# Optimization experiments

Measured on AMD Instinct MI355X. Metric: run time of the kernel, lower is better.

## Reference

```python
import jax, jax.numpy as jnp
import numpy as np

# MANO prior contact vertex indices (f1+f2+f3+f4+f5+f0 from CMap_loss3)
_F1 = [697,698,699,700,712,713,714,715,737,738,739,740,741,743,744,745,746,748,749,750,753,754,755,756,757,758,759,760,761,762,763,764,765,766,767,768]
_F2 = [46,47,48,49,164,165,166,167,194,195,223,237,238,280,281,298,301,317,320,323,324,325,326,327,328,329,330,331,332,333,340,341,342,343,344,345,346,347,348,349,350,351,352,353,354,355]
_F3 = [356,357,358,359,375,376,386,387,396,397,402,403,413,429,433,434,435,436,437,438,439,440,441,442,443,444,452,453,454,455,456,459,460,461,462,463,464,465,466,467]
_F4 = [468,469,470,471,484,485,486,496,497,506,507,513,514,524,545,546,547,548,549,550,551,552,553,555,563,564,565,566,567,570,572,573,574,575,576,577,578]
_F5 = [580,581,582,583,600,601,602,614,615,624,625,630,631,641,663,664,665,666,667,668,670,672,680,681,682,683,684,686,687,688,689,690,691,692,693,694,695]
_F0 = [73,96,98,99,772,774,775,777]
PRIOR_IDX = np.array(_F1 + _F2 + _F3 + _F4 + _F5 + _F0, dtype=np.int32)


def _sqdist(a, b):
    # a: [B,N,3], b: [B,M,3] -> squared distances [B,N,M] via ||a||^2+||b||^2-2ab
    a2 = jnp.sum(a * a, -1)          # [B,N]
    b2 = jnp.sum(b * b, -1)          # [B,M]
    ab = jnp.einsum('bnd,bmd->bnm', a, b)
    return jnp.maximum(a2[:, :, None] + b2[:, None, :] - 2.0 * ab, 0.0)


def _knn1(src, trg):
    # nearest neighbor (K=1): squared dists + indices, like pytorch3d knn_points
    d2 = _sqdist(src, trg)           # [B,N,M]
    return jnp.min(d2, -1), jnp.argmin(d2, -1)


def _verts_normals(verts, faces):
    # area-weighted vertex normals (pytorch3d verts_normals_packed)
    v0 = verts[:, faces[:, 0]]       # [B,F,3]
    v1 = verts[:, faces[:, 1]]
    v2 = verts[:, faces[:, 2]]
    fn = jnp.cross(v1 - v0, v2 - v0)
    vn = jnp.zeros_like(verts)
    vn = vn.at[:, faces[:, 0]].add(fn).at[:, faces[:, 1]].add(fn).at[:, faces[:, 2]].add(fn)
    return vn / (jnp.linalg.norm(vn, axis=-1, keepdims=True) + 1e-12)


def setup_inputs() -> dict:
    key = jax.random.key(0)
    ks = jax.random.split(key, 8)
    B, N1, V, F, Z, P = 64, 8192, 778, 1538, 64, 61
    scale = 0.1  # keep points in a 0.1 box so contact thresholds (0.005/0.01) fire
    return {
        'obj_xyz': jax.random.uniform(ks[0], (B, N1, 3), jnp.float32) * scale,
        'recon_xyz': jax.random.uniform(ks[1], (B, V, 3), jnp.float32) * scale,
        'gt_xyz': jax.random.uniform(ks[2], (B, V, 3), jnp.float32) * scale,
        'mean': jax.random.normal(ks[3], (B, Z), jnp.float32),
        'log_var': jax.random.normal(ks[4], (B, Z), jnp.float32),
        'recon_param': jax.random.normal(ks[5], (B, P), jnp.float32),
        'x_param': jax.random.normal(ks[6], (B, P), jnp.float32),
        'faces': jax.random.randint(ks[7], (F, 3), 0, V, jnp.int32),
    }


def reference(obj_xyz, recon_xyz, gt_xyz, mean, log_var, recon_param, x_param, faces):
    B = obj_xyz.shape[0]
    fB = jnp.float32(B)

    # KNN from object points to gt / reconstructed hand (squared dists)
    d_gt, _ = _knn1(obj_xyz, gt_xyz)            # [B,N1]
    d_rec, idx_rec = _knn1(obj_xyz, recon_xyz)  # [B,N1], [B,N1]

    # param loss: MSE sum / B
    param_loss = jnp.sum((recon_param - x_param) ** 2) / fB

    # CVAE loss: chamfer (point_reduction='sum', batch_reduction='mean') + KLD
    d2 = _sqdist(recon_xyz, gt_xyz)             # [B,778,778]
    recon_loss = jnp.mean(jnp.sum(jnp.min(d2, -1), -1)) + jnp.mean(jnp.sum(jnp.min(d2, -2), -1))
    KLD = -0.5 * jnp.sum(1.0 + log_var - mean ** 2 - jnp.exp(log_var)) / fB * 10.0
    cvae_loss = recon_loss + KLD

    # CMap_loss3: obj NN distance to prior hand contact verts, masked by cmap
    cmap = d_rec < 0.01 ** 2                    # [B,N1] bool
    prior = recon_xyz[:, PRIOR_IDX, :]          # [B,222,3]
    obj_CD, _ = _knn1(obj_xyz, prior)           # [B,N1]
    n_points = jnp.sum(cmap).astype(jnp.float32)
    cmap_loss = 3000.0 * jnp.sum(jnp.where(cmap, obj_CD, 0.0)) / (fB * n_points)

    # CMap consistency: contact-map overlap ratio
    recon_cmap = jnp.sqrt(d_rec) < 0.005
    gt_cmap = jnp.sqrt(d_gt) < 0.005
    gt_cnum = jnp.sum(gt_cmap).astype(jnp.float32) + 0.0001
    consistency_loss = -5.0 * jnp.sum(recon_cmap & gt_cmap).astype(jnp.float32) / gt_cnum

    # inter-penetration: gather NN hand verts/normals, sign of dot, masked dist sum
    vn = _verts_normals(recon_xyz, faces)                               # [B,778,3]
    nn_v = jnp.take_along_axis(recon_xyz, idx_rec[..., None], axis=1)   # [B,N1,3]
    nn_n = jnp.take_along_axis(vn, idx_rec[..., None], axis=1)          # [B,N1,3]
    interior = jnp.sum((nn_v - obj_xyz) * nn_n, -1) > 0                 # [B,N1]
    penetr_loss = 100.0 * jnp.sum(jnp.where(interior, d_rec, 0.0)) / fB

    a, b, c, d, e = 1.0, 0.1, 1000.0, 10.0, 10.0
    loss = a * cvae_loss + b * param_loss + c * cmap_loss + d * consistency_loss + e * penetr_loss
    return loss
```

## Files before the change

### kernel.cpp

```cpp
#include <hip/hip_runtime.h>
#include <math.h>

#define NB     64
#define N1V    8192
#define NPTS   (NB * N1V)
#define NV     778
#define NVP    780
#define NQ     195
#define SEG1Q  51
#define NFACE  1538
#define NZ     64
#define NPAR   61
#define NPRIOR 204
#define PPT    8
#define BIAS   0.0625f

#define REC_BLOCKS 256
#define GT_BLOCKS  256
#define CH_BLOCKS  128
#define NROLE_BLOCKS (REC_BLOCKS + GT_BLOCKS + CH_BLOCKS)
#define CMB_BLOCKS 64

#define BATCH_F4 2352
#define ACC_OFF (NB * BATCH_F4 * 4)
#define RC_OFF  (ACC_OFF + 16)
#define GC_OFF  (RC_OFF + NPTS / 32)

__device__ __constant__ int c_prior[NPRIOR] = {
  697,698,699,700,712,713,714,715,737,738,739,740,741,743,744,745,746,748,749,750,
  753,754,755,756,757,758,759,760,761,762,763,764,765,766,767,768,
  46,47,48,49,164,165,166,167,194,195,223,237,238,280,281,298,301,317,320,323,
  324,325,326,327,328,329,330,331,332,333,340,341,342,343,344,345,346,347,348,349,
  350,351,352,353,354,355,
  356,357,358,359,375,376,386,387,396,397,402,403,413,429,433,434,435,436,437,438,
  439,440,441,442,443,444,452,453,454,455,456,459,460,461,462,463,464,465,466,467,
  468,469,470,471,484,485,486,496,497,506,507,513,514,524,545,546,547,548,549,550,
  551,552,553,555,563,564,565,566,567,570,572,573,574,575,576,577,578,
  580,581,582,583,600,601,602,614,615,624,625,630,631,641,663,664,665,666,667,668,
  670,672,680,681,682,683,684,686,687,688,689,690,691,692,693,694,695,
  73,96,98,99,772,774,775,777
};

__global__ __launch_bounds__(256) void k_prep(const float* __restrict__ recon,
                                              const float* __restrict__ gt,
                                              const int* __restrict__ faces,
                                              float4* __restrict__ ws4,
                                              float* __restrict__ acc) {
    int b = blockIdx.x, tid = threadIdx.x;
    if (b == 0 && tid < 16) acc[tid] = 0.0f;
    __shared__ float4 s_r[NV];
    __shared__ float s_vnx[NV], s_vny[NV], s_vnz[NV];
    __shared__ unsigned int s_bm[25];
    __shared__ unsigned short s_pre[26];
    __shared__ unsigned short s_perm[NV];

    if (tid < 25) s_bm[tid] = 0u;
    __syncthreads();
    if (tid < NPRIOR) {
        int v = c_prior[tid];
        atomicOr(&s_bm[v >> 5], 1u << (v & 31));
    }
    const float* rb = recon + (size_t)b * NV * 3;
    const float* gb = gt    + (size_t)b * NV * 3;
    float4* gt4   = ws4 + (size_t)b * BATCH_F4;
    float4* rec4p = gt4 + NVP;
    float4* nrm4p = rec4p + NVP;
    for (int j = tid; j < NV; j += 256) {
        float x = rb[3*j], y = rb[3*j+1], z = rb[3*j+2];
        s_r[j] = make_float4(x, y, z, x*x + y*y + z*z + BIAS);
        x = gb[3*j]; y = gb[3*j+1]; z = gb[3*j+2];
        gt4[j] = make_float4(x, y, z, x*x + y*y + z*z);
        s_vnx[j] = 0.0f; s_vny[j] = 0.0f; s_vnz[j] = 0.0f;
    }
    if (tid < 2) gt4[NV + tid] = make_float4(0.f, 0.f, 0.f, 1e30f);
    __syncthreads();
    if (tid == 0) {
        unsigned int run = 0;
        for (int w = 0; w < 25; ++w) { s_pre[w] = (unsigned short)run; run += __popc(s_bm[w]); }
        s_pre[25] = (unsigned short)run;
    }
    __syncthreads();
    for (int j = tid; j < NV; j += 256) {
        int w = j >> 5;
        unsigned int below = s_bm[w] & ((1u << (j & 31)) - 1u);
        int rank = s_pre[w] + __popc(below);
        bool member = (s_bm[w] >> (j & 31)) & 1u;
        int pos = member ? rank : (NPRIOR + (j - rank));
        s_perm[pos] = (unsigned short)j;
    }
    for (int f = tid; f < NFACE; f += 256) {
        int i0 = faces[3*f], i1 = faces[3*f+1], i2 = faces[3*f+2];
        float4 p0 = s_r[i0], p1 = s_r[i1], p2 = s_r[i2];
        float e1x = p1.x - p0.x, e1y = p1.y - p0.y, e1z = p1.z - p0.z;
        float e2x = p2.x - p0.x, e2y = p2.y - p0.y, e2z = p2.z - p0.z;
        float fx = e1y * e2z - e1z * e2y;
        float fy = e1z * e2x - e1x * e2z;
        float fz = e1x * e2y - e1y * e2x;
        atomicAdd(&s_vnx[i0], fx); atomicAdd(&s_vny[i0], fy); atomicAdd(&s_vnz[i0], fz);
        atomicAdd(&s_vnx[i1], fx); atomicAdd(&s_vny[i1], fy); atomicAdd(&s_vnz[i1], fz);
        atomicAdd(&s_vnx[i2], fx); atomicAdd(&s_vny[i2], fy); atomicAdd(&s_vnz[i2], fz);
    }
    __syncthreads();
    for (int j = tid; j < NVP; j += 256) {
        if (j < NV) {
            int src = s_perm[j];
            rec4p[j] = s_r[src];
            float x = s_vnx[src], y = s_vny[src], z = s_vnz[src];
            float inv = 1.0f / (sqrtf(x*x + y*y + z*z) + 1e-12f);
            nrm4p[j] = make_float4(x * inv, y * inv, z * inv, 0.0f);
        } else {
            rec4p[j] = make_float4(0.f, 0.f, 0.f, 1e30f);
            nrm4p[j] = make_float4(0.f, 0.f, 1.f, 0.0f);
        }
    }
}

#define LOAD_PTS(ob)                                                          \
    const float4* ob4 = (const float4*)((ob) + (size_t)tid * 24);             \
    float4 q0 = ob4[0], q1 = ob4[1], q2 = ob4[2],                             \
           q3 = ob4[3], q4 = ob4[4], q5 = ob4[5];                             \
    float px[PPT], py[PPT], pz[PPT];                                          \
    px[0]=q0.x; py[0]=q0.y; pz[0]=q0.z;  px[1]=q0.w; py[1]=q1.x; pz[1]=q1.y;  \
    px[2]=q1.z; py[2]=q1.w; pz[2]=q2.x;  px[3]=q2.y; py[3]=q2.z; pz[3]=q2.w;  \
    px[4]=q3.x; py[4]=q3.y; pz[4]=q3.z;  px[5]=q3.w; py[5]=q4.x; pz[5]=q4.y;  \
    px[6]=q4.z; py[6]=q4.w; pz[6]=q5.x;  px[7]=q5.y; py[7]=q5.z; pz[7]=q5.w;

__global__ __launch_bounds__(256) void k_fused(const float* __restrict__ obj,
                                               const float4* __restrict__ ws4,
                                               float* __restrict__ acc,
                                               unsigned char* __restrict__ rcA,
                                               unsigned char* __restrict__ gcA) {
    __shared__ float4 s_t[NVP];
    __shared__ float s_red[3];
    int tid = threadIdx.x;
    int blk = blockIdx.x;

    if (blk < REC_BLOCKS) {
        int b = blk >> 2, chunk = blk & 3;
        const float4* base = ws4 + (size_t)b * BATCH_F4;
        const float4* rec4p = base + NVP;
        const float4* nrm4p = base + 2 * NVP;
        for (int j = tid; j < NVP; j += 256) s_t[j] = rec4p[j];
        if (tid < 3) s_red[tid] = 0.0f;
        __syncthreads();

        const float* ob = obj + ((size_t)b * N1V + (size_t)chunk * 2048) * 3;
        LOAD_PTS(ob)
        float nax[PPT], nay[PPT], naz[PPT], m[PPT];
        int q[PPT];
#pragma unroll
        for (int i = 0; i < PPT; ++i) {
            nax[i] = -2.0f * px[i]; nay[i] = -2.0f * py[i]; naz[i] = -2.0f * pz[i];
            m[i] = 3.4e38f; q[i] = 0;
        }
        float mp[PPT];
#pragma unroll 1
        for (int jq = 0; jq < SEG1Q; ++jq) {
            int j = 4 * jq;
            float4 t0 = s_t[j], t1 = s_t[j+1], t2 = s_t[j+2], t3 = s_t[j+3];
#pragma unroll
            for (int i = 0; i < PPT; ++i) {
                float d0 = fmaf(nax[i], t0.x, fmaf(nay[i], t0.y, fmaf(naz[i], t0.z, t0.w)));
                float d1 = fmaf(nax[i], t1.x, fmaf(nay[i], t1.y, fmaf(naz[i], t1.z, t1.w)));
                float d2 = fmaf(nax[i], t2.x, fmaf(nay[i], t2.y, fmaf(naz[i], t2.z, t2.w)));
                float d3 = fmaf(nax[i], t3.x, fmaf(nay[i], t3.y, fmaf(naz[i], t3.z, t3.w)));
                float mn = fminf(fminf(fminf(d0, d1), fminf(d2, d3)), m[i]);
                q[i] = (mn < m[i]) ? jq : q[i];
                m[i] = mn;
            }
        }
#pragma unroll
        for (int i = 0; i < PPT; ++i) mp[i] = m[i];
#pragma unroll 1
        for (int jq = SEG1Q; jq < NQ; ++jq) {
            int j = 4 * jq;
            float4 t0 = s_t[j], t1 = s_t[j+1], t2 = s_t[j+2], t3 = s_t[j+3];
#pragma unroll
            for (int i = 0; i < PPT; ++i) {
                float d0 = fmaf(nax[i], t0.x, fmaf(nay[i], t0.y, fmaf(naz[i], t0.z, t0.w)));
                float d1 = fmaf(nax[i], t1.x, fmaf(nay[i], t1.y, fmaf(naz[i], t1.z, t1.w)));
                float d2 = fmaf(nax[i], t2.x, fmaf(nay[i], t2.y, fmaf(naz[i], t2.z, t2.w)));
                float d3 = fmaf(nax[i], t3.x, fmaf(nay[i], t3.y, fmaf(naz[i], t3.z, t3.w)));
                float mn = fminf(fminf(fminf(d0, d1), fminf(d2, d3)), m[i]);
                q[i] = (mn < m[i]) ? jq : q[i];
                m[i] = mn;
            }
        }
        float lS_cmap = 0.0f, lN_cmap = 0.0f, lS_pen = 0.0f;
        unsigned int rcbits = 0;
#pragma unroll
        for (int i = 0; i < PPT; ++i) {
            float a2 = px[i]*px[i] + py[i]*py[i] + pz[i]*pz[i];
            float drec = fmaxf(a2 + (m[i]  - BIAS), 0.0f);
            float dpri = fmaxf(a2 + (mp[i] - BIAS), 0.0f);
            bool cm = drec < 1e-4f;
            bool rc = sqrtf(drec) < 0.005f;
            if (cm) { lS_cmap += dpri; lN_cmap += 1.0f; }
            if (rc) rcbits |= (1u << i);
            int jr = 4 * q[i];
            float4 t0 = s_t[jr], t1 = s_t[jr+1], t2 = s_t[jr+2], t3 = s_t[jr+3];
            float d0 = fmaf(nax[i], t0.x, fmaf(nay[i], t0.y, fmaf(naz[i], t0.z, t0.w)));
            float d1 = fmaf(nax[i], t1.x, fmaf(nay[i], t1.y, fmaf(naz[i], t1.z, t1.w)));
            float d2 = fmaf(nax[i], t2.x, fmaf(nay[i], t2.y, fmaf(naz[i], t2.z, t2.w)));
            float d3 = fmaf(nax[i], t3.x, fmaf(nay[i], t3.y, fmaf(naz[i], t3.z, t3.w)));
            float mmin = fminf(fminf(d0, d1), fminf(d2, d3));
            int off = (d0 == mmin) ? 0 : ((d1 == mmin) ? 1 : ((d2 == mmin) ? 2 : 3));
            int jstar = jr + off;
            float4 tS = s_t[jstar];
            float4 nr = nrm4p[jstar];
            float ddot = (tS.x - px[i]) * nr.x + (tS.y - py[i]) * nr.y
                       + (tS.z - pz[i]) * nr.z;
            if (ddot > 0.0f) lS_pen += drec;
        }
        rcA[(size_t)blk * 256 + tid] = (unsigned char)rcbits;
        atomicAdd(&s_red[0], lS_cmap);
        atomicAdd(&s_red[1], lN_cmap);
        atomicAdd(&s_red[2], lS_pen);
        __syncthreads();
        if (tid == 0) atomicAdd(&acc[3], s_red[0]);
        if (tid == 1) atomicAdd(&acc[4], s_red[1]);
        if (tid == 2) atomicAdd(&acc[7], s_red[2]);
        return;
    }

    if (blk < REC_BLOCKS + GT_BLOCKS) {
        int r = blk - REC_BLOCKS;
        int b = r >> 2, chunk = r & 3;
        const float4* gt4v = ws4 + (size_t)b * BATCH_F4;
        for (int j = tid; j < NVP; j += 256) s_t[j] = gt4v[j];
        if (tid == 0) s_red[0] = 0.0f;
        __syncthreads();

        const float* ob = obj + ((size_t)b * N1V + (size_t)chunk * 2048) * 3;
        LOAD_PTS(ob)
        float nax[PPT], nay[PPT], naz[PPT], mgt[PPT];
#pragma unroll
        for (int i = 0; i < PPT; ++i) {
            nax[i] = -2.0f * px[i]; nay[i] = -2.0f * py[i]; naz[i] = -2.0f * pz[i];
            mgt[i] = 3.4e38f;
        }
#pragma unroll 1
        for (int jq = 0; jq < NQ; ++jq) {
            int j = 4 * jq;
            float4 t0 = s_t[j], t1 = s_t[j+1], t2 = s_t[j+2], t3 = s_t[j+3];
#pragma unroll
            for (int i = 0; i < PPT; ++i) {
                float d0 = fmaf(nax[i], t0.x, fmaf(nay[i], t0.y, fmaf(naz[i], t0.z, t0.w)));
                float d1 = fmaf(nax[i], t1.x, fmaf(nay[i], t1.y, fmaf(naz[i], t1.z, t1.w)));
                float d2 = fmaf(nax[i], t2.x, fmaf(nay[i], t2.y, fmaf(naz[i], t2.z, t2.w)));
                float d3 = fmaf(nax[i], t3.x, fmaf(nay[i], t3.y, fmaf(naz[i], t3.z, t3.w)));
                mgt[i] = fminf(fminf(mgt[i], fminf(d0, d1)), fminf(d2, d3));
            }
        }
        float lN_gt = 0.0f;
        unsigned int gcbits = 0;
#pragma unroll
        for (int i = 0; i < PPT; ++i) {
            float a2 = px[i]*px[i] + py[i]*py[i] + pz[i]*pz[i];
            float dgt = fmaxf(a2 + mgt[i], 0.0f);
            if (sqrtf(dgt) < 0.005f) { lN_gt += 1.0f; gcbits |= (1u << i); }
        }
        gcA[(size_t)r * 256 + tid] = (unsigned char)gcbits;
        atomicAdd(&s_red[0], lN_gt);
        __syncthreads();
        if (tid == 0) atomicAdd(&acc[5], s_red[0]);
        return;
    }

    {
        int c   = blk - (REC_BLOCKS + GT_BLOCKS);
        int b   = c >> 1;
        int dir = c & 1;
        const float4* base = ws4 + (size_t)b * BATCH_F4;
        const float4* srcv = dir ? base : (base + NVP);
        const float4* tgtv = dir ? (base + NVP) : base;
        for (int j = tid; j < NVP; j += 256) s_t[j] = tgtv[j];
        if (tid == 0) s_red[0] = 0.0f;
        __syncthreads();

        const int CPT = 4;
        float nax[CPT], nay[CPT], naz[CPT], a2[CPT], m[CPT];
        bool valid[CPT];
#pragma unroll
        for (int k = 0; k < CPT; ++k) {
            int p = tid + 256 * k;
            valid[k] = (p < NV);
            float4 s = srcv[valid[k] ? p : 0];
            nax[k] = -2.0f * s.x; nay[k] = -2.0f * s.y; naz[k] = -2.0f * s.z;
            a2[k] = s.w;
            m[k] = 3.4e38f;
        }
#pragma unroll 1
        for (int j = 0; j < NVP; j += 4) {
            float4 t0 = s_t[j], t1 = s_t[j+1], t2 = s_t[j+2], t3 = s_t[j+3];
#pragma unroll
            for (int k = 0; k < CPT; ++k) {
                float d0 = fmaf(nax[k], t0.x, fmaf(nay[k], t0.y, fmaf(naz[k], t0.z, t0.w)));
                float d1 = fmaf(nax[k], t1.x, fmaf(nay[k], t1.y, fmaf(naz[k], t1.z, t1.w)));
                float d2 = fmaf(nax[k], t2.x, fmaf(nay[k], t2.y, fmaf(naz[k], t2.z, t2.w)));
                float d3 = fmaf(nax[k], t3.x, fmaf(nay[k], t3.y, fmaf(naz[k], t3.z, t3.w)));
                m[k] = fminf(fminf(m[k], fminf(d0, d1)), fminf(d2, d3));
            }
        }
        float local = 0.0f;
#pragma unroll
        for (int k = 0; k < CPT; ++k)
            if (valid[k]) local += fmaxf(a2[k] + m[k] - BIAS, 0.0f);
        atomicAdd(&s_red[0], local);
        __syncthreads();
        if (tid == 0) atomicAdd(&acc[2], s_red[0]);
    }
}

__global__ __launch_bounds__(256) void k_combine(float* __restrict__ acc,
                                                 const unsigned int* __restrict__ rcW,
                                                 const unsigned int* __restrict__ gcW,
                                                 const float* __restrict__ mean,
                                                 const float* __restrict__ log_var,
                                                 const float* __restrict__ rp,
                                                 const float* __restrict__ xp,
                                                 float* __restrict__ out) {
    int blk = blockIdx.x, tid = threadIdx.x;
    __shared__ float s_red[2];
    __shared__ unsigned int s_ticket;
    if (tid < 2) s_red[tid] = 0.0f;
    __syncthreads();
    int idx = blk * 256 + tid;
    unsigned int rc = rcW[idx], gc = gcW[idx];
    float cnt = (float)__popc(rc & gc);
    atomicAdd(&s_red[0], cnt);
    __syncthreads();
    if (tid == 0) atomicAdd(&acc[6], s_red[0]);
    __threadfence();
    if (tid == 0) s_ticket = atomicAdd((unsigned int*)&acc[15], 1u);
    __syncthreads();

    if (s_ticket == CMB_BLOCKS - 1) {
        if (tid < 2) s_red[tid] = 0.0f;
        __syncthreads();
        float s_param = 0.0f, s_kld = 0.0f;
        for (int i = tid; i < NB * NPAR; i += 256) {
            float d = rp[i] - xp[i];
            s_param += d * d;
        }
        for (int i = tid; i < NB * NZ; i += 256) {
            float m = mean[i], lv = log_var[i];
            s_kld += 1.0f + lv - m * m - expf(lv);
        }
        atomicAdd(&s_red[0], s_param);
        atomicAdd(&s_red[1], s_kld);
        __syncthreads();
        if (tid == 0) {
            const float fB = 64.0f;
            float a2v = atomicAdd(&acc[2], 0.0f);
            float a3  = atomicAdd(&acc[3], 0.0f);
            float a4  = atomicAdd(&acc[4], 0.0f);
            float a5  = atomicAdd(&acc[5], 0.0f);
            float a6  = atomicAdd(&acc[6], 0.0f);
            float a7  = atomicAdd(&acc[7], 0.0f);
            float param_loss  = s_red[0] / fB;
            float KLD         = -0.5f * s_red[1] / fB * 10.0f;
            float recon_loss  = a2v / fB;
            float cmap_loss   = 3000.0f * a3 / (fB * a4);
            float consistency = -5.0f * a6 / (a5 + 0.0001f);
            float penetr      = 100.0f * a7 / fB;
            out[0] = (recon_loss + KLD) + 0.1f * param_loss + 1000.0f * cmap_loss
                   + 10.0f * consistency + 10.0f * penetr;
        }
    }
}

extern "C" void kernel_launch(void* const* d_in, const int* in_sizes, int n_in,
                              void* d_out, int out_size, void* d_ws, size_t ws_size,
                              hipStream_t stream) {
    (void)in_sizes; (void)n_in; (void)out_size; (void)ws_size;
    const float* obj     = (const float*)d_in[0];
    const float* recon   = (const float*)d_in[1];
    const float* gt      = (const float*)d_in[2];
    const float* mean    = (const float*)d_in[3];
    const float* log_var = (const float*)d_in[4];
    const float* rp      = (const float*)d_in[5];
    const float* xp      = (const float*)d_in[6];
    const int*   faces   = (const int*)d_in[7];
    float4* ws4 = (float4*)d_ws;
    float* acc  = (float*)d_ws + ACC_OFF;
    unsigned char* rcA = (unsigned char*)((float*)d_ws + RC_OFF);
    unsigned char* gcA = (unsigned char*)((float*)d_ws + GC_OFF);
    float* out  = (float*)d_out;

    k_prep   <<<NB,           256, 0, stream>>>(recon, gt, faces, ws4, acc);
    k_fused  <<<NROLE_BLOCKS, 256, 0, stream>>>(obj, ws4, acc, rcA, gcA);
    k_combine<<<CMB_BLOCKS,   256, 0, stream>>>(acc, (const unsigned int*)rcA,
                                                (const unsigned int*)gcA,
                                                mean, log_var, rp, xp, out);
}
```

Measured before the change: 197.4 us.

## Fuse prep into main kernel and replace global atomics with per-block partials

Removes the separate prep kernel. Each role block now builds its own permuted recon, gt or chamfer target table, and the rec blocks recompute face normals in shared memory. Global float atomics and the ticketed combine are replaced by per-block partial sums that a single-block tail kernel reduces. This drops one launch and the workspace round-trip. In exchange, normal computation is repeated four times per batch and shared memory per block grows, which may reduce occupancy.

```diff
diff --git a/kernel.cpp b/kernel.cpp
--- a/kernel.cpp
+++ b/kernel.cpp
@@ -18,13 +18,11 @@
 #define REC_BLOCKS 256
 #define GT_BLOCKS  256
 #define CH_BLOCKS  128
-#define NROLE_BLOCKS (REC_BLOCKS + GT_BLOCKS + CH_BLOCKS)
-#define CMB_BLOCKS 64
-
-#define BATCH_F4 2352
-#define ACC_OFF (NB * BATCH_F4 * 4)
-#define RC_OFF  (ACC_OFF + 16)
-#define GC_OFF  (RC_OFF + NPTS / 32)
+#define NROLE (REC_BLOCKS + GT_BLOCKS + CH_BLOCKS)
+
+#define PART_OFF 0
+#define RC_OFF   (NROLE * 4)
+#define GC_OFF   (RC_OFF + 16384)
 
 __device__ __constant__ int c_prior[NPRIOR] = {
   697,698,699,700,712,713,714,715,737,738,739,740,741,743,744,745,746,748,749,750,
@@ -41,80 +39,6 @@
   73,96,98,99,772,774,775,777
 };
 
-__global__ __launch_bounds__(256) void k_prep(const float* __restrict__ recon,
-                                              const float* __restrict__ gt,
-                                              const int* __restrict__ faces,
-                                              float4* __restrict__ ws4,
-                                              float* __restrict__ acc) {
-    int b = blockIdx.x, tid = threadIdx.x;
-    if (b == 0 && tid < 16) acc[tid] = 0.0f;
-    __shared__ float4 s_r[NV];
-    __shared__ float s_vnx[NV], s_vny[NV], s_vnz[NV];
-    __shared__ unsigned int s_bm[25];
-    __shared__ unsigned short s_pre[26];
-    __shared__ unsigned short s_perm[NV];
-
-    if (tid < 25) s_bm[tid] = 0u;
-    __syncthreads();
-    if (tid < NPRIOR) {
-        int v = c_prior[tid];
-        atomicOr(&s_bm[v >> 5], 1u << (v & 31));
-    }
-    const float* rb = recon + (size_t)b * NV * 3;
-    const float* gb = gt    + (size_t)b * NV * 3;
-    float4* gt4   = ws4 + (size_t)b * BATCH_F4;
-    float4* rec4p = gt4 + NVP;
-    float4* nrm4p = rec4p + NVP;
-    for (int j = tid; j < NV; j += 256) {
-        float x = rb[3*j], y = rb[3*j+1], z = rb[3*j+2];
-        s_r[j] = make_float4(x, y, z, x*x + y*y + z*z + BIAS);
-        x = gb[3*j]; y = gb[3*j+1]; z = gb[3*j+2];
-        gt4[j] = make_float4(x, y, z, x*x + y*y + z*z);
-        s_vnx[j] = 0.0f; s_vny[j] = 0.0f; s_vnz[j] = 0.0f;
-    }
-    if (tid < 2) gt4[NV + tid] = make_float4(0.f, 0.f, 0.f, 1e30f);
-    __syncthreads();
-    if (tid == 0) {
-        unsigned int run = 0;
-        for (int w = 0; w < 25; ++w) { s_pre[w] = (unsigned short)run; run += __popc(s_bm[w]); }
-        s_pre[25] = (unsigned short)run;
-    }
-    __syncthreads();
-    for (int j = tid; j < NV; j += 256) {
-        int w = j >> 5;
-        unsigned int below = s_bm[w] & ((1u << (j & 31)) - 1u);
-        int rank = s_pre[w] + __popc(below);
-        bool member = (s_bm[w] >> (j & 31)) & 1u;
-        int pos = member ? rank : (NPRIOR + (j - rank));
-        s_perm[pos] = (unsigned short)j;
-    }
-    for (int f = tid; f < NFACE; f += 256) {
-        int i0 = faces[3*f], i1 = faces[3*f+1], i2 = faces[3*f+2];
-        float4 p0 = s_r[i0], p1 = s_r[i1], p2 = s_r[i2];
-        float e1x = p1.x - p0.x, e1y = p1.y - p0.y, e1z = p1.z - p0.z;
-        float e2x = p2.x - p0.x, e2y = p2.y - p0.y, e2z = p2.z - p0.z;
-        float fx = e1y * e2z - e1z * e2y;
-        float fy = e1z * e2x - e1x * e2z;
-        float fz = e1x * e2y - e1y * e2x;
-        atomicAdd(&s_vnx[i0], fx); atomicAdd(&s_vny[i0], fy); atomicAdd(&s_vnz[i0], fz);
-        atomicAdd(&s_vnx[i1], fx); atomicAdd(&s_vny[i1], fy); atomicAdd(&s_vnz[i1], fz);
-        atomicAdd(&s_vnx[i2], fx); atomicAdd(&s_vny[i2], fy); atomicAdd(&s_vnz[i2], fz);
-    }
-    __syncthreads();
-    for (int j = tid; j < NVP; j += 256) {
-        if (j < NV) {
-            int src = s_perm[j];
-            rec4p[j] = s_r[src];
-            float x = s_vnx[src], y = s_vny[src], z = s_vnz[src];
-            float inv = 1.0f / (sqrtf(x*x + y*y + z*z) + 1e-12f);
-            nrm4p[j] = make_float4(x * inv, y * inv, z * inv, 0.0f);
-        } else {
-            rec4p[j] = make_float4(0.f, 0.f, 0.f, 1e30f);
-            nrm4p[j] = make_float4(0.f, 0.f, 1.f, 0.0f);
-        }
-    }
-}
-
 #define LOAD_PTS(ob)                                                          \
     const float4* ob4 = (const float4*)((ob) + (size_t)tid * 24);             \
     float4 q0 = ob4[0], q1 = ob4[1], q2 = ob4[2],                             \
@@ -125,23 +49,79 @@
     px[4]=q3.x; py[4]=q3.y; pz[4]=q3.z;  px[5]=q3.w; py[5]=q4.x; pz[5]=q4.y;  \
     px[6]=q4.z; py[6]=q4.w; pz[6]=q5.x;  px[7]=q5.y; py[7]=q5.z; pz[7]=q5.w;
 
-__global__ __launch_bounds__(256) void k_fused(const float* __restrict__ obj,
-                                               const float4* __restrict__ ws4,
-                                               float* __restrict__ acc,
-                                               unsigned char* __restrict__ rcA,
-                                               unsigned char* __restrict__ gcA) {
+__global__ __launch_bounds__(256) void k_all(const float* __restrict__ obj,
+                                             const float* __restrict__ recon,
+                                             const float* __restrict__ gt,
+                                             const int* __restrict__ faces,
+                                             float* __restrict__ part,
+                                             unsigned char* __restrict__ rcA,
+                                             unsigned char* __restrict__ gcA) {
     __shared__ float4 s_t[NVP];
-    __shared__ float s_red[3];
+    __shared__ float s_vnx[NV], s_vny[NV], s_vnz[NV];
+    __shared__ unsigned short s_perm[NV];
+    __shared__ unsigned int s_bm[25];
+    __shared__ unsigned short s_pre[26];
+    __shared__ float s_red[4];
     int tid = threadIdx.x;
     int blk = blockIdx.x;
 
     if (blk < REC_BLOCKS) {
         int b = blk >> 2, chunk = blk & 3;
-        const float4* base = ws4 + (size_t)b * BATCH_F4;
-        const float4* rec4p = base + NVP;
-        const float4* nrm4p = base + 2 * NVP;
-        for (int j = tid; j < NVP; j += 256) s_t[j] = rec4p[j];
-        if (tid < 3) s_red[tid] = 0.0f;
+        const float* rb = recon + (size_t)b * NV * 3;
+
+        if (tid < 25) s_bm[tid] = 0u;
+        if (tid < 4) s_red[tid] = 0.0f;
+        for (int j = tid; j < NV; j += 256) {
+            s_vnx[j] = 0.0f; s_vny[j] = 0.0f; s_vnz[j] = 0.0f;
+        }
+        __syncthreads();
+        if (tid < NPRIOR) {
+            int v = c_prior[tid];
+            atomicOr(&s_bm[v >> 5], 1u << (v & 31));
+        }
+        __syncthreads();
+        if (tid == 0) {
+            unsigned int run = 0;
+            for (int w = 0; w < 25; ++w) { s_pre[w] = (unsigned short)run; run += __popc(s_bm[w]); }
+            s_pre[25] = (unsigned short)run;
+        }
+        __syncthreads();
+        for (int j = tid; j < NV; j += 256) {
+            int w = j >> 5;
+            unsigned int below = s_bm[w] & ((1u << (j & 31)) - 1u);
+            int rank = s_pre[w] + __popc(below);
+            bool member = (s_bm[w] >> (j & 31)) & 1u;
+            int pos = member ? rank : (NPRIOR + (j - rank));
+            s_perm[pos] = (unsigned short)j;
+        }
+        __syncthreads();
+        for (int j = tid; j < NVP; j += 256) {
+            if (j < NV) {
+                int src = s_perm[j];
+                float x = rb[3*src], y = rb[3*src+1], z = rb[3*src+2];
+                s_t[j] = make_float4(x, y, z, x*x + y*y + z*z + BIAS);
+            } else {
+                s_t[j] = make_float4(0.f, 0.f, 0.f, 1e30f);
+            }
+        }
+        for (int f = tid; f < NFACE; f += 256) {
+            int i0 = faces[3*f], i1 = faces[3*f+1], i2 = faces[3*f+2];
+            float p0x = rb[3*i0], p0y = rb[3*i0+1], p0z = rb[3*i0+2];
+            float e1x = rb[3*i1]   - p0x, e1y = rb[3*i1+1] - p0y, e1z = rb[3*i1+2] - p0z;
+            float e2x = rb[3*i2]   - p0x, e2y = rb[3*i2+1] - p0y, e2z = rb[3*i2+2] - p0z;
+            float fx = e1y * e2z - e1z * e2y;
+            float fy = e1z * e2x - e1x * e2z;
+            float fz = e1x * e2y - e1y * e2x;
+            atomicAdd(&s_vnx[i0], fx); atomicAdd(&s_vny[i0], fy); atomicAdd(&s_vnz[i0], fz);
+            atomicAdd(&s_vnx[i1], fx); atomicAdd(&s_vny[i1], fy); atomicAdd(&s_vnz[i1], fz);
+            atomicAdd(&s_vnx[i2], fx); atomicAdd(&s_vny[i2], fy); atomicAdd(&s_vnz[i2], fz);
+        }
+        __syncthreads();
+        for (int j = tid; j < NV; j += 256) {
+            float x = s_vnx[j], y = s_vny[j], z = s_vnz[j];
+            float inv = 1.0f / (sqrtf(x*x + y*y + z*z) + 1e-12f);
+            s_vnx[j] = x * inv; s_vny[j] = y * inv; s_vnz[j] = z * inv;
+        }
         __syncthreads();
 
         const float* ob = obj + ((size_t)b * N1V + (size_t)chunk * 2048) * 3;
@@ -207,9 +187,9 @@
             int off = (d0 == mmin) ? 0 : ((d1 == mmin) ? 1 : ((d2 == mmin) ? 2 : 3));
             int jstar = jr + off;
             float4 tS = s_t[jstar];
-            float4 nr = nrm4p[jstar];
-            float ddot = (tS.x - px[i]) * nr.x + (tS.y - py[i]) * nr.y
-                       + (tS.z - pz[i]) * nr.z;
+            int jo = s_perm[jstar];
+            float ddot = (tS.x - px[i]) * s_vnx[jo] + (tS.y - py[i]) * s_vny[jo]
+                       + (tS.z - pz[i]) * s_vnz[jo];
             if (ddot > 0.0f) lS_pen += drec;
         }
         rcA[(size_t)blk * 256 + tid] = (unsigned char)rcbits;
@@ -217,17 +197,25 @@
         atomicAdd(&s_red[1], lN_cmap);
         atomicAdd(&s_red[2], lS_pen);
         __syncthreads();
-        if (tid == 0) atomicAdd(&acc[3], s_red[0]);
-        if (tid == 1) atomicAdd(&acc[4], s_red[1]);
-        if (tid == 2) atomicAdd(&acc[7], s_red[2]);
+        if (tid < 4) {
+            float v = (tid < 3) ? s_red[tid] : 0.0f;
+            part[(size_t)blk * 4 + tid] = v;
+        }
         return;
     }
 
     if (blk < REC_BLOCKS + GT_BLOCKS) {
         int r = blk - REC_BLOCKS;
         int b = r >> 2, chunk = r & 3;
-        const float4* gt4v = ws4 + (size_t)b * BATCH_F4;
-        for (int j = tid; j < NVP; j += 256) s_t[j] = gt4v[j];
+        const float* gb = gt + (size_t)b * NV * 3;
+        for (int j = tid; j < NVP; j += 256) {
+            if (j < NV) {
+                float x = gb[3*j], y = gb[3*j+1], z = gb[3*j+2];
+                s_t[j] = make_float4(x, y, z, x*x + y*y + z*z);
+            } else {
+                s_t[j] = make_float4(0.f, 0.f, 0.f, 1e30f);
+            }
+        }
         if (tid == 0) s_red[0] = 0.0f;
         __syncthreads();
 
@@ -263,7 +251,7 @@
         gcA[(size_t)r * 256 + tid] = (unsigned char)gcbits;
         atomicAdd(&s_red[0], lN_gt);
         __syncthreads();
-        if (tid == 0) atomicAdd(&acc[5], s_red[0]);
+        if (tid < 4) part[(size_t)blk * 4 + tid] = (tid == 0) ? s_red[0] : 0.0f;
         return;
     }
 
@@ -271,10 +259,18 @@
         int c   = blk - (REC_BLOCKS + GT_BLOCKS);
         int b   = c >> 1;
         int dir = c & 1;
-        const float4* base = ws4 + (size_t)b * BATCH_F4;
-        const float4* srcv = dir ? base : (base + NVP);
-        const float4* tgtv = dir ? (base + NVP) : base;
-        for (int j = tid; j < NVP; j += 256) s_t[j] = tgtv[j];
+        const float* sbase = (dir ? gt : recon) + (size_t)b * NV * 3;
+        const float* tbase = (dir ? recon : gt) + (size_t)b * NV * 3;
+        float tb_bias = dir ? BIAS : 0.0f;
+        float sb_bias = dir ? 0.0f : BIAS;
+        for (int j = tid; j < NVP; j += 256) {
+            if (j < NV) {
+                float x = tbase[3*j], y = tbase[3*j+1], z = tbase[3*j+2];
+                s_t[j] = make_float4(x, y, z, x*x + y*y + z*z + tb_bias);
+            } else {
+                s_t[j] = make_float4(0.f, 0.f, 0.f, 1e30f);
+            }
+        }
         if (tid == 0) s_red[0] = 0.0f;
         __syncthreads();
 
@@ -285,9 +281,10 @@
         for (int k = 0; k < CPT; ++k) {
             int p = tid + 256 * k;
             valid[k] = (p < NV);
-            float4 s = srcv[valid[k] ? p : 0];
-            nax[k] = -2.0f * s.x; nay[k] = -2.0f * s.y; naz[k] = -2.0f * s.z;
-            a2[k] = s.w;
+            int pp = valid[k] ? p : 0;
+            float x = sbase[3*pp], y = sbase[3*pp+1], z = sbase[3*pp+2];
+            nax[k] = -2.0f * x; nay[k] = -2.0f * y; naz[k] = -2.0f * z;
+            a2[k] = x*x + y*y + z*z + sb_bias;
             m[k] = 3.4e38f;
         }
 #pragma unroll 1
@@ -308,65 +305,60 @@
             if (valid[k]) local += fmaxf(a2[k] + m[k] - BIAS, 0.0f);
         atomicAdd(&s_red[0], local);
         __syncthreads();
-        if (tid == 0) atomicAdd(&acc[2], s_red[0]);
+        if (tid < 4) part[(size_t)blk * 4 + tid] = (tid == 0) ? s_red[0] : 0.0f;
     }
 }
 
-__global__ __launch_bounds__(256) void k_combine(float* __restrict__ acc,
-                                                 const unsigned int* __restrict__ rcW,
-                                                 const unsigned int* __restrict__ gcW,
-                                                 const float* __restrict__ mean,
-                                                 const float* __restrict__ log_var,
-                                                 const float* __restrict__ rp,
-                                                 const float* __restrict__ xp,
-                                                 float* __restrict__ out) {
-    int blk = blockIdx.x, tid = threadIdx.x;
-    __shared__ float s_red[2];
-    __shared__ unsigned int s_ticket;
-    if (tid < 2) s_red[tid] = 0.0f;
+__global__ __launch_bounds__(256) void k_tail(const float* __restrict__ part,
+                                              const unsigned int* __restrict__ rcW,
+                                              const unsigned int* __restrict__ gcW,
+                                              const float* __restrict__ mean,
+                                              const float* __restrict__ log_var,
+                                              const float* __restrict__ rp,
+                                              const float* __restrict__ xp,
+                                              float* __restrict__ out) {
+    int tid = threadIdx.x;
+    __shared__ float red[8];
+    if (tid < 8) red[tid] = 0.0f;
     __syncthreads();
-    int idx = blk * 256 + tid;
-    unsigned int rc = rcW[idx], gc = gcW[idx];
-    float cnt = (float)__popc(rc & gc);
-    atomicAdd(&s_red[0], cnt);
+    float l0=0, l1=0, l2=0, l3=0, l4=0;
+    for (int r = tid; r < NROLE; r += 256) {
+        const float* row = part + (size_t)r * 4;
+        if (r < REC_BLOCKS)                 { l0 += row[0]; l1 += row[1]; l2 += row[2]; }
+        else if (r < REC_BLOCKS + GT_BLOCKS){ l3 += row[0]; }
+        else                                { l4 += row[0]; }
+    }
+    float l5 = 0.0f;
+    for (int i = tid; i < 16384; i += 256)
+        l5 += (float)__popc(rcW[i] & gcW[i]);
+    float s_param = 0.0f, s_kld = 0.0f;
+    for (int i = tid; i < NB * NPAR; i += 256) {
+        float d = rp[i] - xp[i];
+        s_param += d * d;
+    }
+    for (int i = tid; i < NB * NZ; i += 256) {
+        float m = mean[i], lv = log_var[i];
+        s_kld += 1.0f + lv - m * m - expf(lv);
+    }
+    atomicAdd(&red[0], l0);
+    atomicAdd(&red[1], l1);
+    atomicAdd(&red[2], l2);
+    atomicAdd(&red[3], l3);
+    atomicAdd(&red[4], l4);
+    atomicAdd(&red[5], l5);
+    atomicAdd(&red[6], s_param);
+    atomicAdd(&red[7], s_kld);
     __syncthreads();
-    if (tid == 0) atomicAdd(&acc[6], s_red[0]);
-    __threadfence();
-    if (tid == 0) s_ticket = atomicAdd((unsigned int*)&acc[15], 1u);
-    __syncthreads();
-
-    if (s_ticket == CMB_BLOCKS - 1) {
-        if (tid < 2) s_red[tid] = 0.0f;
-        __syncthreads();
-        float s_param = 0.0f, s_kld = 0.0f;
-        for (int i = tid; i < NB * NPAR; i += 256) {
-            float d = rp[i] - xp[i];
-            s_param += d * d;
-        }
-        for (int i = tid; i < NB * NZ; i += 256) {
-            float m = mean[i], lv = log_var[i];
-            s_kld += 1.0f + lv - m * m - expf(lv);
-        }
-        atomicAdd(&s_red[0], s_param);
-        atomicAdd(&s_red[1], s_kld);
-        __syncthreads();
-        if (tid == 0) {
-            const float fB = 64.0f;
-            float a2v = atomicAdd(&acc[2], 0.0f);
-            float a3  = atomicAdd(&acc[3], 0.0f);
-            float a4  = atomicAdd(&acc[4], 0.0f);
-            float a5  = atomicAdd(&acc[5], 0.0f);
-            float a6  = atomicAdd(&acc[6], 0.0f);
-            float a7  = atomicAdd(&acc[7], 0.0f);
-            float param_loss  = s_red[0] / fB;
-            float KLD         = -0.5f * s_red[1] / fB * 10.0f;
-            float recon_loss  = a2v / fB;
-            float cmap_loss   = 3000.0f * a3 / (fB * a4);
-            float consistency = -5.0f * a6 / (a5 + 0.0001f);
-            float penetr      = 100.0f * a7 / fB;
-            out[0] = (recon_loss + KLD) + 0.1f * param_loss + 1000.0f * cmap_loss
-                   + 10.0f * consistency + 10.0f * penetr;
-        }
+    if (tid == 0) {
+        const float fB = 64.0f;
+        float param_loss  = red[6] / fB;
+        float KLD         = -0.5f * red[7] / fB * 10.0f;
+        float recon_loss  = red[4] / fB;
+        float cmap_loss   = 3000.0f * red[0] / (fB * red[1]);
+        float consistency = -5.0f * red[5] / (red[3] + 0.0001f);
+        float penetr      = 100.0f * red[2] / fB;
+        out[0] = (recon_loss + KLD) + 0.1f * param_loss + 1000.0f * cmap_loss
+               + 10.0f * consistency + 10.0f * penetr;
     }
 }
 
@@ -382,15 +374,13 @@
     const float* rp      = (const float*)d_in[5];
     const float* xp      = (const float*)d_in[6];
     const int*   faces   = (const int*)d_in[7];
-    float4* ws4 = (float4*)d_ws;
-    float* acc  = (float*)d_ws + ACC_OFF;
+    float* part = (float*)d_ws + PART_OFF;
     unsigned char* rcA = (unsigned char*)((float*)d_ws + RC_OFF);
     unsigned char* gcA = (unsigned char*)((float*)d_ws + GC_OFF);
     float* out  = (float*)d_out;
 
-    k_prep   <<<NB,           256, 0, stream>>>(recon, gt, faces, ws4, acc);
-    k_fused  <<<NROLE_BLOCKS, 256, 0, stream>>>(obj, ws4, acc, rcA, gcA);
-    k_combine<<<CMB_BLOCKS,   256, 0, stream>>>(acc, (const unsigned int*)rcA,
-                                                (const unsigned int*)gcA,
-                                                mean, log_var, rp, xp, out);
+    k_all <<<NROLE, 256, 0, stream>>>(obj, recon, gt, faces, part, rcA, gcA);
+    k_tail<<<1,     256, 0, stream>>>(part, (const unsigned int*)rcA,
+                                      (const unsigned int*)gcA,
+                                      mean, log_var, rp, xp, out);
 }
```

After: 207.9 us. 1.05x slower.
